# Kernel tuning notes

Measured on AMD Instinct MI355X. Metric: run time of the kernel, lower is better.

## Reference

```python
import jax, jax.numpy as jnp
import numpy as np

# ---- static config (mirrors TALoss(num_classes=80, reg_max=16, strides=[8,16,32])) ----
B, M, NC, REG_MAX = 32, 20, 80, 16
STRIDES = (8, 16, 32)
HW = ((80, 80), (40, 40), (20, 20))          # feature map sizes for 640x640 input
NO = REG_MAX * 4 + NC                         # 144 channels per head
A = sum(h * w for h, w in HW)                 # 8400 anchors
TOPK, ALPHA, BETA = 10, 0.5, 6.0
BOX_G, CLS_G, DFL_G = 7.5, 0.5, 1.5
EPS = 1e-9


def setup_inputs() -> dict:
    key = jax.random.key(0)
    ks = jax.random.split(key, 6)
    feats = {f"feat{i}": jax.random.normal(ks[i], (B, NO, h, w), jnp.float32)
             for i, (h, w) in enumerate(HW)}
    # targets: (N,6) rows of (img_idx, class, cx, cy, w, h), normalized, 20 boxes/image, sorted by image
    img_idx = jnp.repeat(jnp.arange(B, dtype=jnp.float32), M)
    cls = jax.random.randint(ks[3], (B * M,), 0, NC).astype(jnp.float32)
    cxy = jax.random.uniform(ks[4], (B * M, 2), minval=0.2, maxval=0.8)
    wh = jax.random.uniform(ks[5], (B * M, 2), minval=0.05, maxval=0.3)
    targets = jnp.concatenate([img_idx[:, None], cls[:, None], cxy, wh], axis=1)
    return {**feats, "targets": targets}


def _make_anchors():
    pts, strs = [], []
    for (h, w), s in zip(HW, STRIDES):
        sx = jnp.arange(w, dtype=jnp.float32) + 0.5
        sy = jnp.arange(h, dtype=jnp.float32) + 0.5
        gy, gx = jnp.meshgrid(sy, sx, indexing="ij")
        pts.append(jnp.stack([gx, gy], -1).reshape(-1, 2))
        strs.append(jnp.full((h * w, 1), float(s), jnp.float32))
    return jnp.concatenate(pts), jnp.concatenate(strs)   # (A,2), (A,1)


def _ciou(b1, b2, eps=1e-7):
    # b1, b2: broadcastable xyxy boxes (..., 4) -> CIoU (...,)
    b1x1, b1y1, b1x2, b1y2 = b1[..., 0], b1[..., 1], b1[..., 2], b1[..., 3]
    b2x1, b2y1, b2x2, b2y2 = b2[..., 0], b2[..., 1], b2[..., 2], b2[..., 3]
    w1, h1 = b1x2 - b1x1, b1y2 - b1y1 + eps
    w2, h2 = b2x2 - b2x1, b2y2 - b2y1 + eps
    inter = (jnp.clip(jnp.minimum(b1x2, b2x2) - jnp.maximum(b1x1, b2x1), 0)
             * jnp.clip(jnp.minimum(b1y2, b2y2) - jnp.maximum(b1y1, b2y1), 0))
    union = w1 * h1 + w2 * h2 - inter + eps
    iou = inter / union
    cw = jnp.maximum(b1x2, b2x2) - jnp.minimum(b1x1, b2x1)
    ch = jnp.maximum(b1y2, b2y2) - jnp.minimum(b1y1, b2y1)
    c2 = cw ** 2 + ch ** 2 + eps
    rho2 = ((b2x1 + b2x2 - b1x1 - b1x2) ** 2 + (b2y1 + b2y2 - b1y1 - b1y2) ** 2) / 4.0
    v = (4.0 / np.pi ** 2) * (jnp.arctan(w2 / h2) - jnp.arctan(w1 / h1)) ** 2
    a = jax.lax.stop_gradient(v / (v - iou + (1.0 + eps)))   # torch: computed under no_grad
    return iou - (rho2 / c2 + v * a)


def _assign(pd_scores, pd_bboxes, anc, gt_labels, gt_bboxes, mask_gt):
    """TaskAlignedAssigner. pd_scores (B,A,NC) sigmoid-ed, pd_bboxes (B,A,4) image units,
    anc (A,2) image units, gt_labels (B,M), gt_bboxes (B,M,4), mask_gt (B,M) float."""
    # anchors inside each gt box -> (B,M,A)
    lt = anc[None, None, :, :] - gt_bboxes[:, :, None, :2]
    rb = gt_bboxes[:, :, None, 2:] - anc[None, None, :, :]
    mask_in = (jnp.concatenate([lt, rb], -1).min(-1) > EPS).astype(jnp.float32)
    mask = mask_in * mask_gt[..., None]                      # (B,M,A) candidate mask
    overlaps = jnp.clip(_ciou(gt_bboxes[:, :, None, :], pd_bboxes[:, None, :, :]), 0) * mask
    labels = gt_labels.astype(jnp.int32)                     # (B,M)
    # scores of each gt's class at every anchor: (B,M,A)
    bbox_scores = jnp.take_along_axis(pd_scores.transpose(0, 2, 1),
                                      jnp.broadcast_to(labels[:, :, None], (B, M, A)), axis=1) * mask
    align = (bbox_scores ** ALPHA) * (overlaps ** BETA)      # (B,M,A), already zero off-mask
    # top-k anchors per gt
    _, idxs = jax.lax.top_k(align, TOPK)                     # (B,M,K)
    idxs = jnp.where(mask_gt[..., None] > 0, idxs, 0)
    cnt = jax.nn.one_hot(idxs, A, dtype=jnp.float32).sum(-2)  # (B,M,A)
    mask_topk = jnp.where(cnt > 1, 0.0, cnt)
    mask_pos = mask_topk * mask
    # resolve anchors matched to multiple gts: keep the max-overlap gt
    fg = mask_pos.sum(1)                                     # (B,A)
    is_max = jnp.moveaxis(jax.nn.one_hot(overlaps.argmax(1), M, dtype=jnp.float32), -1, 1)  # (B,M,A)
    mask_pos = jnp.where(fg[:, None, :] > 1, is_max, mask_pos)
    fg = mask_pos.sum(1)
    tgt_idx = mask_pos.argmax(1)                             # (B,A)
    t_labels = jnp.take_along_axis(labels, tgt_idx, 1)       # (B,A)
    t_bboxes = jnp.take_along_axis(gt_bboxes, tgt_idx[..., None], 1)  # (B,A,4)
    fg_b = (fg > 0).astype(jnp.float32)
    t_scores = jax.nn.one_hot(t_labels, NC, dtype=jnp.float32) * fg_b[..., None]
    # normalize scores: align * (max overlap per gt) / (max align per gt)
    align_pos = align * mask_pos
    pos_align = align_pos.max(-1, keepdims=True)             # (B,M,1)
    pos_over = (overlaps * mask_pos).max(-1, keepdims=True)
    norm = (align_pos * pos_over / (pos_align + EPS)).max(1)  # (B,A)
    return t_bboxes, t_scores * norm[..., None], fg_b


def _forward(feat0, feat1, feat2, targets):
    feats = [feat0, feat1, feat2]
    pred = jnp.concatenate([f.reshape(B, NO, -1) for f in feats], axis=2)
    pred_distri = pred[:, :REG_MAX * 4].transpose(0, 2, 1)   # (B,A,64)
    pred_scores = pred[:, REG_MAX * 4:].transpose(0, 2, 1)   # (B,A,NC)
    anc, stride_t = _make_anchors()
    img_h, img_w = HW[0][0] * STRIDES[0], HW[0][1] * STRIDES[0]
    scale = jnp.array([img_w, img_h, img_w, img_h], jnp.float32)
    # ---- preprocess targets (N,6) -> padded (B,M,5), xywh*scale -> xyxy ----
    idx = targets[:, 0].astype(jnp.int32)
    pos = jnp.arange(targets.shape[0]) - jnp.searchsorted(idx, idx, side="left")
    out = jnp.zeros((B, M, 5), jnp.float32).at[idx, pos].set(targets[:, 1:])
    gt_labels = out[..., 0]
    xywh = out[..., 1:5] * scale
    gt_bboxes = jnp.concatenate([xywh[..., :2] - xywh[..., 2:] / 2,
                                 xywh[..., :2] + xywh[..., 2:] / 2], -1)
    mask_gt = (gt_bboxes.sum(-1) > 0).astype(jnp.float32)    # (B,M)
    # ---- DFL bbox decode (feature-map units) ----
    proj = jnp.arange(REG_MAX, dtype=jnp.float32)
    dist = jax.nn.softmax(pred_distri.reshape(B, A, 4, REG_MAX), -1) @ proj  # (B,A,4) ltrb
    pred_bboxes = jnp.concatenate([anc - dist[..., :2], anc + dist[..., 2:]], -1)
    # ---- task-aligned assignment (on detached preds, image units) ----
    pd_scores = jax.lax.stop_gradient(jax.nn.sigmoid(pred_scores))
    pd_bboxes = jax.lax.stop_gradient(pred_bboxes) * stride_t
    target_bboxes, target_scores, fg_mask = _assign(pd_scores, pd_bboxes, anc * stride_t,
                                                    gt_labels, gt_bboxes, mask_gt)
    target_bboxes = target_bboxes / stride_t
    tss = jnp.maximum(target_scores.sum(), 1.0)
    # ---- BCE-with-logits classification loss (pos_weight=1) ----
    x, t = pred_scores, target_scores
    bce = jnp.maximum(x, 0) - x * t + jnp.log1p(jnp.exp(-jnp.abs(x)))
    loss_cls = bce.sum() / tss
    # ---- CIoU box loss + DFL, weighted by per-anchor target score sum on fg ----
    weight = target_scores.sum(-1) * fg_mask                 # (B,A)
    iou = _ciou(pred_bboxes, target_bboxes)
    loss_box = ((1.0 - iou) * weight).sum() / tss
    tltrb = jnp.clip(jnp.concatenate([anc - target_bboxes[..., :2],
                                      target_bboxes[..., 2:] - anc], -1),
                     0, REG_MAX - 1 - 0.01)                  # (B,A,4)
    logp = jax.nn.log_softmax(pred_distri.reshape(B, A, 4, REG_MAX), -1)
    tl = tltrb.astype(jnp.int32)
    wl = (tl + 1).astype(jnp.float32) - tltrb
    nll_l = -jnp.take_along_axis(logp, tl[..., None], -1)[..., 0]
    nll_r = -jnp.take_along_axis(logp, (tl + 1)[..., None], -1)[..., 0]
    dfl = (nll_l * wl + nll_r * (1.0 - wl)).mean(-1)         # (B,A)
    loss_dfl = (dfl * weight).sum() / tss
    losses = jnp.stack([loss_box * BOX_G, loss_cls * CLS_G, loss_dfl * DFL_G])
    return losses.sum() * B, jax.lax.stop_gradient(losses)


def reference(feat0, feat1, feat2, targets):
    return _forward(feat0, feat1, feat2, targets)
```

## Files before the change

### kernel.cpp

```cpp
#include <hip/hip_runtime.h>
#include <math.h>

constexpr int BB  = 32;
constexpr int MM  = 20;
constexpr int NCC = 80;
constexpr int RM  = 16;
constexpr int NOC = 144;
constexpr int AT  = 8400;
constexpr int TK  = 10;
constexpr int BA  = BB * AT;
constexpr int BM  = BB * MM;
constexpr int MAXPOS = BM * TK;
constexpr int NSLOT = 1024;
constexpr float EPS_A = 1e-9f;
constexpr float VCOEF = 0.40528473456935108577551785283891f;

constexpr int TPI    = 34;
constexpr int NTILES = BB * TPI;

struct Lvl { const float* f; int o, w, hw; float s; };

__device__ inline Lvl level_of(int a, const float* f0, const float* f1, const float* f2){
  Lvl L;
  if (a < 6400)      { L.f = f0; L.o = a;        L.w = 80; L.hw = 6400; L.s = 8.f;  }
  else if (a < 8000) { L.f = f1; L.o = a - 6400; L.w = 40; L.hw = 1600; L.s = 16.f; }
  else               { L.f = f2; L.o = a - 8000; L.w = 20; L.hw = 400;  L.s = 32.f; }
  return L;
}

__device__ inline float frcp(float x){ return __builtin_amdgcn_rcpf(x); }

__device__ inline float fast_atan(float x){
  float ax = fabsf(x);
  bool big = ax > 1.f;
  float z = big ? frcp(ax) : ax;
  float z2 = z * z;
  float p = fmaf(z2, -0.0117212f, 0.0526533f);
  p = fmaf(z2, p, -0.1164329f);
  p = fmaf(z2, p, 0.1935435f);
  p = fmaf(z2, p, -0.3326235f);
  p = fmaf(z2, p, 0.9999773f);
  float r = z * p;
  r = big ? 1.57079632679f - r : r;
  return copysignf(r, x);
}

__device__ inline float ciou_f(float b1x1,float b1y1,float b1x2,float b1y2,
                               float b2x1,float b2y1,float b2x2,float b2y2){
  const float eps = 1e-7f;
  float w1 = b1x2 - b1x1, h1 = b1y2 - b1y1 + eps;
  float w2 = b2x2 - b2x1, h2 = b2y2 - b2y1 + eps;
  float iw = fmaxf(fminf(b1x2, b2x2) - fmaxf(b1x1, b2x1), 0.f);
  float ih = fmaxf(fminf(b1y2, b2y2) - fmaxf(b1y1, b2y1), 0.f);
  float inter = iw * ih;
  float uni = w1 * h1 + w2 * h2 - inter + eps;
  float iou = inter * frcp(uni);
  float cw = fmaxf(b1x2, b2x2) - fminf(b1x1, b2x1);
  float ch = fmaxf(b1y2, b2y2) - fminf(b1y1, b2y1);
  float c2 = cw * cw + ch * ch + eps;
  float dx = b2x1 + b2x2 - b1x1 - b1x2;
  float dy = b2y1 + b2y2 - b1y1 - b1y2;
  float rho2 = (dx * dx + dy * dy) * 0.25f;
  float r1 = w1 * frcp(h1), r2 = w2 * frcp(h2);
  float dat = fast_atan((r2 - r1) * frcp(fmaf(r1, r2, 1.f)));
  float v = VCOEF * dat * dat;
  float alpha = v * frcp(v - iou + (1.0f + eps));
  return iou - (rho2 * frcp(c2) + v * alpha);
}

__device__ inline unsigned long long shfl_xor_u64(unsigned long long v, int mask){
  int lo = __shfl_xor((int)(unsigned)(v & 0xFFFFFFFFull), mask);
  int hi = __shfl_xor((int)(unsigned)(v >> 32), mask);
  return ((unsigned long long)(unsigned)hi << 32) | (unsigned)lo;
}

__device__ inline float softplus4(float4 v){
  float s = fmaxf(v.x, 0.f) + __logf(1.f + __expf(-fabsf(v.x)));
  s += fmaxf(v.y, 0.f) + __logf(1.f + __expf(-fabsf(v.y)));
  s += fmaxf(v.z, 0.f) + __logf(1.f + __expf(-fabsf(v.z)));
  s += fmaxf(v.w, 0.f) + __logf(1.f + __expf(-fabsf(v.w)));
  return s;
}

template<int NA, int HW, int W, int AOFF>
__device__ inline float feat_tile(const float* __restrict__ f, int b, int o0,
                                  float* __restrict__ sT,
                                  float4* __restrict__ pbox,
                                  float4* __restrict__ lse,
                                  unsigned* __restrict__ mpos){
  constexpr int NA4  = NA / 4;
  constexpr int NDF4 = 64 * NA4;
  constexpr int NIT  = NDF4 / 256;
  int tid = threadIdx.x;
  const float* base = f + (size_t)b * NOC * HW + o0;

  {
    float4 x[NIT];
#pragma unroll
    for (int k = 0; k < NIT; k++){
      int idx = k * 256 + tid;
      int ch = idx / NA4, pos = idx - ch * NA4;
      x[k] = *(const float4*)(base + (size_t)ch * HW + pos * 4);
    }
#pragma unroll
    for (int k = 0; k < NIT; k++){
      int idx = k * 256 + tid;
      int ch = idx / NA4, pos = idx - ch * NA4;
      *(float4*)(&sT[ch * NA + pos * 4]) = x[k];
    }
  }
  __syncthreads();

  if (tid < NA){
    float d[4], ls[4];
#pragma unroll
    for (int s = 0; s < 4; s++){
      float xs[16];
#pragma unroll
      for (int j = 0; j < 16; j++) xs[j] = sT[(s * 16 + j) * NA + tid];
      float mx = xs[0];
#pragma unroll
      for (int j = 1; j < 16; j++) mx = fmaxf(mx, xs[j]);
      float sm = 0.f, dt = 0.f;
#pragma unroll
      for (int j = 0; j < 16; j++){
        float e = __expf(xs[j] - mx);
        sm += e; dt = fmaf(e, (float)j, dt);
      }
      d[s]  = dt * frcp(sm);
      ls[s] = mx + __logf(sm);
    }
    int o = o0 + tid;
    int iy = o / W;
    float ax = (float)(o - iy * W) + 0.5f;
    float ay = (float)iy + 0.5f;
    int gi = b * AT + AOFF + o;
    pbox[gi] = make_float4(ax - d[0], ay - d[1], ax + d[2], ay + d[3]);
    lse[gi]  = make_float4(ls[0], ls[1], ls[2], ls[3]);
    mpos[gi] = 0u;
  }

  const float* cbase = base + (size_t)(4 * RM) * HW;
  constexpr int NCF4 = 80 * NA4;
  constexpr int NKC  = NCF4 / 256;
  float sp = 0.f;
#pragma unroll
  for (int k = 0; k < NKC; k++){
    int idx = k * 256 + tid;
    int ch = idx / NA4, pos = idx - ch * NA4;
    sp += softplus4(*(const float4*)(cbase + (size_t)ch * HW + pos * 4));
  }
  if constexpr (NCF4 % 256 != 0){
    int idx = NKC * 256 + tid;
    if (idx < NCF4){
      int ch = idx / NA4, pos = idx - ch * NA4;
      sp += softplus4(*(const float4*)(cbase + (size_t)ch * HW + pos * 4));
    }
  }
  return sp;
}

__global__ __launch_bounds__(256) void k_feat6(
    const float* __restrict__ f0, const float* __restrict__ f1,
    const float* __restrict__ f2, const float* __restrict__ tgt,
    float4* __restrict__ pbox, float4* __restrict__ lse,
    unsigned* __restrict__ mpos, double* __restrict__ bce_part,
    float* __restrict__ out5, float* __restrict__ gtbox,
    int* __restrict__ gtlab, float* __restrict__ gtmask,
    int* __restrict__ pa_i, int* __restrict__ po_i,
    int* __restrict__ topk_arr, double* __restrict__ acc){
  __shared__ float sT[64 * 256];
  __shared__ float red[4];
  int blk = blockIdx.x;
  int tid = threadIdx.x;
  if (blk < NTILES){
    int b = blk / TPI, tt = blk - b * TPI;
    float sp;
    if (tt < 25)       sp = feat_tile<256, 6400, 80, 0>   (f0, b, tt * 256,        sT, pbox, lse, mpos);
    else if (tt < 31)  sp = feat_tile<256, 1600, 40, 6400>(f1, b, (tt - 25) * 256, sT, pbox, lse, mpos);
    else if (tt == 31) sp = feat_tile< 64, 1600, 40, 6400>(f1, b, 1536,            sT, pbox, lse, mpos);
    else if (tt == 32) sp = feat_tile<256,  400, 20, 8000>(f2, b, 0,               sT, pbox, lse, mpos);
    else               sp = feat_tile<144,  400, 20, 8000>(f2, b, 256,             sT, pbox, lse, mpos);
    for (int off = 32; off; off >>= 1) sp += __shfl_down(sp, off);
    int wid = tid >> 6, lid = tid & 63;
    if (lid == 0) red[wid] = sp;
    __syncthreads();
    if (tid == 0) bce_part[blk] = (double)(red[0] + red[1] + red[2] + red[3]);
  } else {
    for (int i = tid; i < BM * 5; i += 256) out5[i] = 0.f;
    for (int i = tid; i < MAXPOS; i += 256) topk_arr[i] = -1;
    for (int i = tid; i < BM; i += 256){ pa_i[i] = 0; po_i[i] = 0; }
    if (tid < 8) acc[tid] = 0.0;
    __syncthreads();
    for (int t = tid; t < BM; t += 256){
      int img = (int)tgt[t * 6 + 0];
      int j = t;
      while (j > 0 && (int)tgt[(j - 1) * 6 + 0] == img) j--;
      int pos = t - j;
      if (img >= 0 && img < BB && pos < MM){
        for (int k = 0; k < 5; k++)
          out5[(img * MM + pos) * 5 + k] = tgt[t * 6 + 1 + k];
      }
    }
    __syncthreads();
    for (int t = tid; t < BM; t += 256){
      float lab = out5[t * 5 + 0];
      float cx = out5[t * 5 + 1] * 640.f;
      float cy = out5[t * 5 + 2] * 640.f;
      float w  = out5[t * 5 + 3] * 640.f;
      float h  = out5[t * 5 + 4] * 640.f;
      float x1 = cx - w * 0.5f, y1 = cy - h * 0.5f;
      float x2 = cx + w * 0.5f, y2 = cy + h * 0.5f;
      gtbox[t * 4 + 0] = x1; gtbox[t * 4 + 1] = y1;
      gtbox[t * 4 + 2] = x2; gtbox[t * 4 + 3] = y2;
      gtlab[t] = (int)lab;
      gtmask[t] = ((x1 + y1 + x2 + y2) > 0.f) ? 1.f : 0.f;
    }
  }
}

__global__ __launch_bounds__(256) void k_align(
    const float* __restrict__ f0, const float* __restrict__ f1,
    const float* __restrict__ f2, const float4* __restrict__ pbox,
    const float* __restrict__ gtbox, const int* __restrict__ gtlab,
    const float* __restrict__ gtmask,
    unsigned* __restrict__ mpos, int* __restrict__ topk_arr){
  int pair = blockIdx.x;
  int b = pair / MM, m = pair % MM;
  if (gtmask[pair] <= 0.f) return;
  int tid = threadIdx.x;
  float gx1 = gtbox[pair * 4 + 0], gy1 = gtbox[pair * 4 + 1];
  float gx2 = gtbox[pair * 4 + 2], gy2 = gtbox[pair * 4 + 3];
  int lab = gtlab[pair];
  __shared__ float s_val[NSLOT];
  __shared__ int   s_anc[NSLOT];
  __shared__ unsigned long long s_red[4];
  __shared__ int   s_win[TK];
  int base = 0;

#define PROC_LEVEL(FPTR, W, HW, AOFF, S)                                      \
  {                                                                           \
    const float s_ = (S); const float inv_ = 1.f / (S);                       \
    int x0 = max(0, (int)floorf(gx1 * inv_ - 0.5f));                          \
    int x1 = min((W) - 1, (int)ceilf(gx2 * inv_ - 0.5f));                     \
    int y0 = max(0, (int)floorf(gy1 * inv_ - 0.5f));                          \
    int y1 = min((W) - 1, (int)ceilf(gy2 * inv_ - 0.5f));                     \
    int nxx = x1 - x0 + 1, nyy = y1 - y0 + 1;                                 \
    if (nxx > 0 && nyy > 0){                                                  \
      int ntot = nxx * nyy;                                                   \
      unsigned magic = 0xFFFFFFFFu / (unsigned)nxx + 1u;                      \
      const float* clsrow = (FPTR) + (size_t)b * NOC * (HW)                   \
                            + (size_t)(4 * RM + lab) * (HW);                  \
      for (int t = tid; t < ntot; t += 256){                                  \
        int slot = base + t;                                                  \
        if (slot >= NSLOT) break;                                             \
        int iy = (int)(((unsigned long long)(unsigned)t * magic) >> 32);      \
        int ix = t - iy * nxx + x0;                                           \
        iy += y0;                                                             \
        float ax = ((float)ix + 0.5f) * s_;                                   \
        float ay = ((float)iy + 0.5f) * s_;                                   \
        float mn = fminf(fminf(ax - gx1, ay - gy1),                           \
                         fminf(gx2 - ax, gy2 - ay));                          \
        int o = iy * (W) + ix;                                                \
        int a = (AOFF) + o;                                                   \
        float aln = -1.f;                                                     \
        if (mn > EPS_A){                                                      \
          float4 pb = pbox[b * AT + a];                                       \
          float c = ciou_f(gx1, gy1, gx2, gy2,                                \
                           pb.x * s_, pb.y * s_, pb.z * s_, pb.w * s_);       \
          float ovl = fmaxf(c, 0.f);                                          \
          if (ovl > 0.f){                                                     \
            float xv = clsrow[o];                                             \
            float sc = frcp(1.f + __expf(-xv));                               \
            float o2 = ovl * ovl;                                             \
            aln = sqrtf(sc) * (o2 * o2 * o2);                                 \
          }                                                                   \
        }                                                                     \
        s_val[slot] = aln;                                                    \
        s_anc[slot] = a;                                                      \
      }                                                                       \
      base += ntot;                                                           \
    }                                                                         \
  }

  PROC_LEVEL(f0, 80, 6400, 0, 8.f)
  PROC_LEVEL(f1, 40, 1600, 6400, 16.f)
  PROC_LEVEL(f2, 20, 400, 8000, 32.f)
#undef PROC_LEVEL

  __syncthreads();
  int total = min(base, NSLOT);
  int wid = tid >> 6, lid = tid & 63;
  for (int r = 0; r < TK; r++){
    unsigned long long key = 0ULL;
    for (int i = tid; i < total; i += 256){
      float v = s_val[i];
      if (v > 0.f){
        unsigned long long k2 =
            ((unsigned long long)__float_as_uint(v) << 32) |
            (unsigned long long)(0xFFFFFFFFu - (unsigned)i);
        key = key > k2 ? key : k2;
      }
    }
    for (int xm = 1; xm < 64; xm <<= 1){
      unsigned long long o = shfl_xor_u64(key, xm);
      key = key > o ? key : o;
    }
    if (lid == 0) s_red[wid] = key;
    __syncthreads();
    if (tid == 0){
      unsigned long long k = s_red[0];
      k = k > s_red[1] ? k : s_red[1];
      k = k > s_red[2] ? k : s_red[2];
      k = k > s_red[3] ? k : s_red[3];
      if (k){
        int slot = (int)(0xFFFFFFFFu - (unsigned)(k & 0xFFFFFFFFull));
        s_win[r] = s_anc[slot];
        s_val[slot] = -1.f;
      } else s_win[r] = -1;
    }
    __syncthreads();
  }
  if (tid < TK){
    int a = s_win[tid];
    topk_arr[pair * TK + tid] = a;
    if (a >= 0) atomicOr(&mpos[(size_t)b * AT + a], 1u << m);
  }
}

__global__ __launch_bounds__(256) void k_resolve(
    const float* __restrict__ f0, const float* __restrict__ f1,
    const float* __restrict__ f2, const float4* __restrict__ pbox,
    const float* __restrict__ gtbox, const int* __restrict__ gtlab,
    const float* __restrict__ gtmask, const unsigned* __restrict__ mpos,
    const int* __restrict__ topk_arr,
    unsigned char* __restrict__ resm, float* __restrict__ resaln,
    int* __restrict__ pa_i, int* __restrict__ po_i){
  int i = blockIdx.x * 256 + threadIdx.x;
  int a = topk_arr[i];
  if (a < 0) return;
  int pair = i / TK;
  int b = pair / MM, m = pair % MM;
  unsigned bits = mpos[(size_t)b * AT + a];
  if (m != __ffs(bits) - 1) return;
  Lvl L = level_of(a, f0, f1, f2);
  float ax = ((float)(L.o % L.w) + 0.5f) * L.s;
  float ay = ((float)(L.o / L.w) + 0.5f) * L.s;
  float4 pb = pbox[b * AT + a];
  float px1 = pb.x * L.s, py1 = pb.y * L.s, px2 = pb.z * L.s, py2 = pb.w * L.s;
  int mr; float ovl;
  if (__popc(bits) > 1){
    float best = -1.f; int bm = 0;
    for (int mm = 0; mm < MM; mm++){
      float v = 0.f;
      if (gtmask[b * MM + mm] > 0.f){
        float x1 = gtbox[(b * MM + mm) * 4 + 0], y1 = gtbox[(b * MM + mm) * 4 + 1];
        float x2 = gtbox[(b * MM + mm) * 4 + 2], y2 = gtbox[(b * MM + mm) * 4 + 3];
        float mn = fminf(fminf(ax - x1, ay - y1), fminf(x2 - ax, y2 - ay));
        if (mn > EPS_A)
          v = fmaxf(ciou_f(x1, y1, x2, y2, px1, py1, px2, py2), 0.f);
      }
      if (v > best){ best = v; bm = mm; }
    }
    mr = bm; ovl = fmaxf(best, 0.f);
  } else {
    mr = m;
    float x1 = gtbox[(b * MM + mr) * 4 + 0], y1 = gtbox[(b * MM + mr) * 4 + 1];
    float x2 = gtbox[(b * MM + mr) * 4 + 2], y2 = gtbox[(b * MM + mr) * 4 + 3];
    ovl = fmaxf(ciou_f(x1, y1, x2, y2, px1, py1, px2, py2), 0.f);
  }
  int lab = gtlab[b * MM + mr];
  float xv = L.f[(size_t)b * NOC * L.hw + (size_t)(4 * RM + lab) * L.hw + L.o];
  float sc = frcp(1.f + __expf(-xv));
  float o2 = ovl * ovl;
  float aln = sqrtf(sc) * (o2 * o2 * o2);
  size_t gi = (size_t)b * AT + a;
  resm[gi] = (unsigned char)mr;
  resaln[gi] = aln;
  atomicMax(&pa_i[b * MM + mr], __float_as_int(aln));
  atomicMax(&po_i[b * MM + mr], __float_as_int(ovl));
}

__global__ __launch_bounds__(256) void k_final(
    const float* __restrict__ f0, const float* __restrict__ f1,
    const float* __restrict__ f2,
    const float4* __restrict__ pbox, const float4* __restrict__ lse,
    const float* __restrict__ gtbox, const int* __restrict__ gtlab,
    const int* __restrict__ pa_i, const int* __restrict__ po_i,
    const unsigned* __restrict__ mpos, const int* __restrict__ topk_arr,
    const unsigned char* __restrict__ resm, const float* __restrict__ resaln,
    double* __restrict__ acc){
  int i = blockIdx.x * 256 + threadIdx.x;
  float w_ = 0.f, clsp = 0.f, boxp = 0.f, dflp = 0.f;
  int a = topk_arr[i];
  if (a >= 0){
    int pair = i / TK;
    int b = pair / MM, m = pair % MM;
    unsigned bits = mpos[(size_t)b * AT + a];
    if (m == __ffs(bits) - 1){
      size_t gi = (size_t)b * AT + a;
      int mr = (int)resm[gi];
      float aln = resaln[gi];
      float pa = __int_as_float(pa_i[b * MM + mr]);
      float po = __int_as_float(po_i[b * MM + mr]);
      w_ = aln * po * frcp(pa + EPS_A);
      Lvl L = level_of(a, f0, f1, f2);
      const float* base = L.f + (size_t)b * NOC * L.hw + L.o;
      float ax = (float)(L.o % L.w) + 0.5f;
      float ay = (float)(L.o / L.w) + 0.5f;
      float inv_s = frcp(L.s);
      float tx1 = gtbox[(b * MM + mr) * 4 + 0] * inv_s, ty1 = gtbox[(b * MM + mr) * 4 + 1] * inv_s;
      float tx2 = gtbox[(b * MM + mr) * 4 + 2] * inv_s, ty2 = gtbox[(b * MM + mr) * 4 + 3] * inv_s;
      float4 pb = pbox[b * AT + a];
      float iou = ciou_f(pb.x, pb.y, pb.z, pb.w, tx1, ty1, tx2, ty2);
      boxp = (1.f - iou) * w_;
      float4 L4 = lse[b * AT + a];
      float lsv[4] = { L4.x, L4.y, L4.z, L4.w };
      float tv[4] = { ax - tx1, ay - ty1, tx2 - ax, ty2 - ay };
      float dfl = 0.f;
#pragma unroll
      for (int s4 = 0; s4 < 4; s4++){
        float t = fminf(fmaxf(tv[s4], 0.f), (float)(RM - 1) - 0.01f);
        int tl = (int)t;
        float wl = (float)(tl + 1) - t;
        float xl = base[(size_t)(s4 * RM + tl) * L.hw];
        float xr = base[(size_t)(s4 * RM + tl + 1) * L.hw];
        dfl += (lsv[s4] - xl) * wl + (lsv[s4] - xr) * (1.f - wl);
      }
      dflp = dfl * 0.25f * w_;
      int lab = gtlab[b * MM + mr];
      clsp = base[(size_t)(4 * RM + lab) * L.hw] * w_;
    }
  }
  __shared__ float red[4][4];
  float vals[4] = { w_, clsp, boxp, dflp };
  int wid = threadIdx.x >> 6, lid = threadIdx.x & 63;
#pragma unroll
  for (int j = 0; j < 4; j++){
    float v = vals[j];
    for (int off = 32; off; off >>= 1) v += __shfl_down(v, off);
    if (lid == 0) red[wid][j] = v;
  }
  __syncthreads();
  if (threadIdx.x == 0){
    float t0 = 0.f, t1 = 0.f, t2 = 0.f, t3 = 0.f;
    for (int w2 = 0; w2 < 4; w2++){
      t0 += red[w2][0]; t1 += red[w2][1]; t2 += red[w2][2]; t3 += red[w2][3];
    }
    atomicAdd(&acc[0], (double)t0);
    atomicAdd(&acc[1], (double)t1);
    atomicAdd(&acc[2], (double)t2);
    atomicAdd(&acc[3], (double)t3);
  }
}

__global__ void k_out(const double* __restrict__ acc,
                      const double* __restrict__ bce_part,
                      float* __restrict__ out){
  __shared__ double sd[256];
  double s = 0.0;
  for (int i = threadIdx.x; i < NTILES; i += 256) s += bce_part[i];
  sd[threadIdx.x] = s;
  __syncthreads();
  for (int off = 128; off; off >>= 1){
    if (threadIdx.x < off) sd[threadIdx.x] += sd[threadIdx.x + off];
    __syncthreads();
  }
  if (threadIdx.x == 0){
    double bce_sum = sd[0];
    double tss = acc[0] > 1.0 ? acc[0] : 1.0;
    double loss_box = acc[2] / tss;
    double loss_cls = (bce_sum - acc[1]) / tss;
    double loss_dfl = acc[3] / tss;
    float l0 = (float)(loss_box * 7.5);
    float l1 = (float)(loss_cls * 0.5);
    float l2 = (float)(loss_dfl * 1.5);
    out[0] = (l0 + l1 + l2) * 32.f;
    out[1] = l0;
    out[2] = l1;
    out[3] = l2;
  }
}

extern "C" void kernel_launch(void* const* d_in, const int* in_sizes, int n_in,
                              void* d_out, int out_size, void* d_ws, size_t ws_size,
                              hipStream_t stream) {
  const float* f0 = (const float*)d_in[0];
  const float* f1 = (const float*)d_in[1];
  const float* f2 = (const float*)d_in[2];
  const float* tg = (const float*)d_in[3];
  float* out = (float*)d_out;

  char* w = (char*)d_ws;
  size_t off = 0;
  auto alloc = [&](size_t bytes) -> void* {
    void* p = w + off;
    off += (bytes + 255) & ~(size_t)255;
    return p;
  };
  float4*        pbox    = (float4*)       alloc((size_t)BA * 16);
  float4*        lse     = (float4*)       alloc((size_t)BA * 16);
  float*         gtbox   = (float*)        alloc((size_t)BM * 16);
  int*           gtlab   = (int*)          alloc((size_t)BM * 4);
  float*         gtmask  = (float*)        alloc((size_t)BM * 4);
  float*         out5    = (float*)        alloc((size_t)BM * 20);
  unsigned*      mpos    = (unsigned*)     alloc((size_t)BA * 4);
  int*           topk_arr= (int*)          alloc((size_t)MAXPOS * 4);
  unsigned char* resm    = (unsigned char*)alloc((size_t)BA);
  float*         resaln  = (float*)        alloc((size_t)BA * 4);
  int*           pa      = (int*)          alloc((size_t)BM * 4);
  int*           po      = (int*)          alloc((size_t)BM * 4);
  double*        acc     = (double*)       alloc(8 * 8);
  double*        bcep    = (double*)       alloc((size_t)NTILES * 8);

  k_feat6<<<NTILES + 1, 256, 0, stream>>>(f0, f1, f2, tg, pbox, lse, mpos, bcep,
                                          out5, gtbox, gtlab, gtmask, pa, po,
                                          topk_arr, acc);
  k_align<<<BM, 256, 0, stream>>>(f0, f1, f2, pbox, gtbox, gtlab, gtmask, mpos, topk_arr);
  k_resolve<<<MAXPOS / 256, 256, 0, stream>>>(f0, f1, f2, pbox, gtbox, gtlab, gtmask,
                                              mpos, topk_arr, resm, resaln, pa, po);
  k_final<<<MAXPOS / 256, 256, 0, stream>>>(f0, f1, f2, pbox, lse, gtbox, gtlab,
                                            pa, po, mpos, topk_arr, resm, resaln, acc);
  k_out<<<1, 256, 0, stream>>>(acc, bcep, out);
}
```

Baseline: 248.5 us.

## Fuse align, resolve, final and output kernels into one persistent kernel with grid barriers

```diff
diff --git a/kernel.cpp b/kernel.cpp
--- a/kernel.cpp
+++ b/kernel.cpp
@@ -168,7 +168,7 @@
     float* __restrict__ out5, float* __restrict__ gtbox,
     int* __restrict__ gtlab, float* __restrict__ gtmask,
     int* __restrict__ pa_i, int* __restrict__ po_i,
-    int* __restrict__ topk_arr, double* __restrict__ acc){
+    int* __restrict__ topk_arr, int* __restrict__ bar){
   __shared__ float sT[64 * 256];
   __shared__ float red[4];
   int blk = blockIdx.x;
@@ -190,7 +190,7 @@
     for (int i = tid; i < BM * 5; i += 256) out5[i] = 0.f;
     for (int i = tid; i < MAXPOS; i += 256) topk_arr[i] = -1;
     for (int i = tid; i < BM; i += 256){ pa_i[i] = 0; po_i[i] = 0; }
-    if (tid < 8) acc[tid] = 0.0;
+    if (tid < 8) bar[tid] = 0;
     __syncthreads();
     for (int t = tid; t < BM; t += 256){
       int img = (int)tgt[t * 6 + 0];
@@ -219,24 +219,46 @@
   }
 }
 
-__global__ __launch_bounds__(256) void k_align(
+__device__ inline void grid_barrier(int* bar, int phase, int nblk){
+  __syncthreads();
+  if (threadIdx.x == 0){
+    __threadfence();
+    atomicAdd(&bar[phase], 1);
+    while (__hip_atomic_load(&bar[phase], __ATOMIC_ACQUIRE,
+                             __HIP_MEMORY_SCOPE_AGENT) < nblk){
+      __builtin_amdgcn_s_sleep(8);
+    }
+    __threadfence();
+  }
+  __syncthreads();
+}
+
+__global__ __launch_bounds__(256, 4) void k_tail(
     const float* __restrict__ f0, const float* __restrict__ f1,
     const float* __restrict__ f2, const float4* __restrict__ pbox,
+    const float4* __restrict__ lse,
     const float* __restrict__ gtbox, const int* __restrict__ gtlab,
     const float* __restrict__ gtmask,
-    unsigned* __restrict__ mpos, int* __restrict__ topk_arr){
-  int pair = blockIdx.x;
-  int b = pair / MM, m = pair % MM;
-  if (gtmask[pair] <= 0.f) return;
-  int tid = threadIdx.x;
-  float gx1 = gtbox[pair * 4 + 0], gy1 = gtbox[pair * 4 + 1];
-  float gx2 = gtbox[pair * 4 + 2], gy2 = gtbox[pair * 4 + 3];
-  int lab = gtlab[pair];
+    unsigned* __restrict__ mpos, int* __restrict__ topk_arr,
+    int* __restrict__ pa_i, int* __restrict__ po_i,
+    const double* __restrict__ bce_part, float* __restrict__ fpart,
+    int* __restrict__ bar, float* __restrict__ out){
   __shared__ float s_val[NSLOT];
   __shared__ int   s_anc[NSLOT];
   __shared__ unsigned long long s_red[4];
   __shared__ int   s_win[TK];
-  int base = 0;
+  __shared__ double sd[256];
+  __shared__ double res[5];
+
+  int pair = blockIdx.x;
+  int b = pair / MM, m = pair % MM;
+  int tid = threadIdx.x;
+
+  if (gtmask[pair] > 0.f){
+    float gx1 = gtbox[pair * 4 + 0], gy1 = gtbox[pair * 4 + 1];
+    float gx2 = gtbox[pair * 4 + 2], gy2 = gtbox[pair * 4 + 3];
+    int lab = gtlab[pair];
+    int base = 0;
 
 #define PROC_LEVEL(FPTR, W, HW, AOFF, S)                                      \
   {                                                                           \
@@ -283,129 +305,109 @@
     }                                                                         \
   }
 
-  PROC_LEVEL(f0, 80, 6400, 0, 8.f)
-  PROC_LEVEL(f1, 40, 1600, 6400, 16.f)
-  PROC_LEVEL(f2, 20, 400, 8000, 32.f)
+    PROC_LEVEL(f0, 80, 6400, 0, 8.f)
+    PROC_LEVEL(f1, 40, 1600, 6400, 16.f)
+    PROC_LEVEL(f2, 20, 400, 8000, 32.f)
 #undef PROC_LEVEL
 
-  __syncthreads();
-  int total = min(base, NSLOT);
-  int wid = tid >> 6, lid = tid & 63;
-  for (int r = 0; r < TK; r++){
-    unsigned long long key = 0ULL;
-    for (int i = tid; i < total; i += 256){
-      float v = s_val[i];
-      if (v > 0.f){
-        unsigned long long k2 =
-            ((unsigned long long)__float_as_uint(v) << 32) |
-            (unsigned long long)(0xFFFFFFFFu - (unsigned)i);
-        key = key > k2 ? key : k2;
-      }
-    }
-    for (int xm = 1; xm < 64; xm <<= 1){
-      unsigned long long o = shfl_xor_u64(key, xm);
-      key = key > o ? key : o;
-    }
-    if (lid == 0) s_red[wid] = key;
     __syncthreads();
-    if (tid == 0){
-      unsigned long long k = s_red[0];
-      k = k > s_red[1] ? k : s_red[1];
-      k = k > s_red[2] ? k : s_red[2];
-      k = k > s_red[3] ? k : s_red[3];
-      if (k){
-        int slot = (int)(0xFFFFFFFFu - (unsigned)(k & 0xFFFFFFFFull));
-        s_win[r] = s_anc[slot];
-        s_val[slot] = -1.f;
-      } else s_win[r] = -1;
-    }
-    __syncthreads();
-  }
+    int total = min(base, NSLOT);
+    int wid = tid >> 6, lid = tid & 63;
+    for (int r = 0; r < TK; r++){
+      unsigned long long key = 0ULL;
+      for (int i = tid; i < total; i += 256){
+        float v = s_val[i];
+        if (v > 0.f){
+          unsigned long long k2 =
+              ((unsigned long long)__float_as_uint(v) << 32) |
+              (unsigned long long)(0xFFFFFFFFu - (unsigned)i);
+          key = key > k2 ? key : k2;
+        }
+      }
+      for (int xm = 1; xm < 64; xm <<= 1){
+        unsigned long long o = shfl_xor_u64(key, xm);
+        key = key > o ? key : o;
+      }
+      if (lid == 0) s_red[wid] = key;
+      __syncthreads();
+      if (tid == 0){
+        unsigned long long k = s_red[0];
+        k = k > s_red[1] ? k : s_red[1];
+        k = k > s_red[2] ? k : s_red[2];
+        k = k > s_red[3] ? k : s_red[3];
+        if (k){
+          int slot = (int)(0xFFFFFFFFu - (unsigned)(k & 0xFFFFFFFFull));
+          s_win[r] = s_anc[slot];
+          s_val[slot] = -1.f;
+        } else s_win[r] = -1;
+      }
+      __syncthreads();
+    }
+    if (tid < TK){
+      int a = s_win[tid];
+      topk_arr[pair * TK + tid] = a;
+      if (a >= 0) atomicOr(&mpos[(size_t)b * AT + a], 1u << m);
+    }
+  }
+  grid_barrier(bar, 0, BM);
+
+  bool owner = false;
+  int a_own = -1, mr = 0;
+  float aln_own = 0.f;
   if (tid < TK){
-    int a = s_win[tid];
-    topk_arr[pair * TK + tid] = a;
-    if (a >= 0) atomicOr(&mpos[(size_t)b * AT + a], 1u << m);
-  }
-}
-
-__global__ __launch_bounds__(256) void k_resolve(
-    const float* __restrict__ f0, const float* __restrict__ f1,
-    const float* __restrict__ f2, const float4* __restrict__ pbox,
-    const float* __restrict__ gtbox, const int* __restrict__ gtlab,
-    const float* __restrict__ gtmask, const unsigned* __restrict__ mpos,
-    const int* __restrict__ topk_arr,
-    unsigned char* __restrict__ resm, float* __restrict__ resaln,
-    int* __restrict__ pa_i, int* __restrict__ po_i){
-  int i = blockIdx.x * 256 + threadIdx.x;
-  int a = topk_arr[i];
-  if (a < 0) return;
-  int pair = i / TK;
-  int b = pair / MM, m = pair % MM;
-  unsigned bits = mpos[(size_t)b * AT + a];
-  if (m != __ffs(bits) - 1) return;
-  Lvl L = level_of(a, f0, f1, f2);
-  float ax = ((float)(L.o % L.w) + 0.5f) * L.s;
-  float ay = ((float)(L.o / L.w) + 0.5f) * L.s;
-  float4 pb = pbox[b * AT + a];
-  float px1 = pb.x * L.s, py1 = pb.y * L.s, px2 = pb.z * L.s, py2 = pb.w * L.s;
-  int mr; float ovl;
-  if (__popc(bits) > 1){
-    float best = -1.f; int bm = 0;
-    for (int mm = 0; mm < MM; mm++){
-      float v = 0.f;
-      if (gtmask[b * MM + mm] > 0.f){
-        float x1 = gtbox[(b * MM + mm) * 4 + 0], y1 = gtbox[(b * MM + mm) * 4 + 1];
-        float x2 = gtbox[(b * MM + mm) * 4 + 2], y2 = gtbox[(b * MM + mm) * 4 + 3];
-        float mn = fminf(fminf(ax - x1, ay - y1), fminf(x2 - ax, y2 - ay));
-        if (mn > EPS_A)
-          v = fmaxf(ciou_f(x1, y1, x2, y2, px1, py1, px2, py2), 0.f);
-      }
-      if (v > best){ best = v; bm = mm; }
-    }
-    mr = bm; ovl = fmaxf(best, 0.f);
-  } else {
-    mr = m;
-    float x1 = gtbox[(b * MM + mr) * 4 + 0], y1 = gtbox[(b * MM + mr) * 4 + 1];
-    float x2 = gtbox[(b * MM + mr) * 4 + 2], y2 = gtbox[(b * MM + mr) * 4 + 3];
-    ovl = fmaxf(ciou_f(x1, y1, x2, y2, px1, py1, px2, py2), 0.f);
-  }
-  int lab = gtlab[b * MM + mr];
-  float xv = L.f[(size_t)b * NOC * L.hw + (size_t)(4 * RM + lab) * L.hw + L.o];
-  float sc = frcp(1.f + __expf(-xv));
-  float o2 = ovl * ovl;
-  float aln = sqrtf(sc) * (o2 * o2 * o2);
-  size_t gi = (size_t)b * AT + a;
-  resm[gi] = (unsigned char)mr;
-  resaln[gi] = aln;
-  atomicMax(&pa_i[b * MM + mr], __float_as_int(aln));
-  atomicMax(&po_i[b * MM + mr], __float_as_int(ovl));
-}
-
-__global__ __launch_bounds__(256) void k_final(
-    const float* __restrict__ f0, const float* __restrict__ f1,
-    const float* __restrict__ f2,
-    const float4* __restrict__ pbox, const float4* __restrict__ lse,
-    const float* __restrict__ gtbox, const int* __restrict__ gtlab,
-    const int* __restrict__ pa_i, const int* __restrict__ po_i,
-    const unsigned* __restrict__ mpos, const int* __restrict__ topk_arr,
-    const unsigned char* __restrict__ resm, const float* __restrict__ resaln,
-    double* __restrict__ acc){
-  int i = blockIdx.x * 256 + threadIdx.x;
-  float w_ = 0.f, clsp = 0.f, boxp = 0.f, dflp = 0.f;
-  int a = topk_arr[i];
-  if (a >= 0){
-    int pair = i / TK;
-    int b = pair / MM, m = pair % MM;
-    unsigned bits = mpos[(size_t)b * AT + a];
-    if (m == __ffs(bits) - 1){
-      size_t gi = (size_t)b * AT + a;
-      int mr = (int)resm[gi];
-      float aln = resaln[gi];
+    int i = pair * TK + tid;
+    int a = topk_arr[i];
+    if (a >= 0){
+      unsigned bits = mpos[(size_t)b * AT + a];
+      if (m == __ffs(bits) - 1){
+        owner = true; a_own = a;
+        Lvl L = level_of(a, f0, f1, f2);
+        float ax = ((float)(L.o % L.w) + 0.5f) * L.s;
+        float ay = ((float)(L.o / L.w) + 0.5f) * L.s;
+        float4 pb = pbox[b * AT + a];
+        float px1 = pb.x * L.s, py1 = pb.y * L.s, px2 = pb.z * L.s, py2 = pb.w * L.s;
+        float ovl;
+        if (__popc(bits) > 1){
+          float best = -1.f; int bm = 0;
+          for (int mm = 0; mm < MM; mm++){
+            float v = 0.f;
+            if (gtmask[b * MM + mm] > 0.f){
+              float x1 = gtbox[(b * MM + mm) * 4 + 0], y1 = gtbox[(b * MM + mm) * 4 + 1];
+              float x2 = gtbox[(b * MM + mm) * 4 + 2], y2 = gtbox[(b * MM + mm) * 4 + 3];
+              float mn = fminf(fminf(ax - x1, ay - y1), fminf(x2 - ax, y2 - ay));
+              if (mn > EPS_A)
+                v = fmaxf(ciou_f(x1, y1, x2, y2, px1, py1, px2, py2), 0.f);
+            }
+            if (v > best){ best = v; bm = mm; }
+          }
+          mr = bm; ovl = fmaxf(best, 0.f);
+        } else {
+          mr = m;
+          float x1 = gtbox[(b * MM + mr) * 4 + 0], y1 = gtbox[(b * MM + mr) * 4 + 1];
+          float x2 = gtbox[(b * MM + mr) * 4 + 2], y2 = gtbox[(b * MM + mr) * 4 + 3];
+          ovl = fmaxf(ciou_f(x1, y1, x2, y2, px1, py1, px2, py2), 0.f);
+        }
+        int lab = gtlab[b * MM + mr];
+        float xv = L.f[(size_t)b * NOC * L.hw + (size_t)(4 * RM + lab) * L.hw + L.o];
+        float sc = frcp(1.f + __expf(-xv));
+        float o2 = ovl * ovl;
+        aln_own = sqrtf(sc) * (o2 * o2 * o2);
+        atomicMax(&pa_i[b * MM + mr], __float_as_int(aln_own));
+        atomicMax(&po_i[b * MM + mr], __float_as_int(ovl));
+      }
+    }
+  }
+  grid_barrier(bar, 1, BM);
+
+  {
+    float w_ = 0.f, clsp = 0.f, boxp = 0.f, dflp = 0.f;
+    if (owner){
+      int a = a_own;
       float pa = __int_as_float(pa_i[b * MM + mr]);
       float po = __int_as_float(po_i[b * MM + mr]);
-      w_ = aln * po * frcp(pa + EPS_A);
+      w_ = aln_own * po * frcp(pa + EPS_A);
       Lvl L = level_of(a, f0, f1, f2);
-      const float* base = L.f + (size_t)b * NOC * L.hw + L.o;
+      const float* base2 = L.f + (size_t)b * NOC * L.hw + L.o;
       float ax = (float)(L.o % L.w) + 0.5f;
       float ay = (float)(L.o / L.w) + 0.5f;
       float inv_s = frcp(L.s);
@@ -423,62 +425,57 @@
         float t = fminf(fmaxf(tv[s4], 0.f), (float)(RM - 1) - 0.01f);
         int tl = (int)t;
         float wl = (float)(tl + 1) - t;
-        float xl = base[(size_t)(s4 * RM + tl) * L.hw];
-        float xr = base[(size_t)(s4 * RM + tl + 1) * L.hw];
+        float xl = base2[(size_t)(s4 * RM + tl) * L.hw];
+        float xr = base2[(size_t)(s4 * RM + tl + 1) * L.hw];
         dfl += (lsv[s4] - xl) * wl + (lsv[s4] - xr) * (1.f - wl);
       }
       dflp = dfl * 0.25f * w_;
       int lab = gtlab[b * MM + mr];
-      clsp = base[(size_t)(4 * RM + lab) * L.hw] * w_;
-    }
-  }
-  __shared__ float red[4][4];
-  float vals[4] = { w_, clsp, boxp, dflp };
-  int wid = threadIdx.x >> 6, lid = threadIdx.x & 63;
-#pragma unroll
-  for (int j = 0; j < 4; j++){
-    float v = vals[j];
-    for (int off = 32; off; off >>= 1) v += __shfl_down(v, off);
-    if (lid == 0) red[wid][j] = v;
-  }
-  __syncthreads();
-  if (threadIdx.x == 0){
-    float t0 = 0.f, t1 = 0.f, t2 = 0.f, t3 = 0.f;
-    for (int w2 = 0; w2 < 4; w2++){
-      t0 += red[w2][0]; t1 += red[w2][1]; t2 += red[w2][2]; t3 += red[w2][3];
-    }
-    atomicAdd(&acc[0], (double)t0);
-    atomicAdd(&acc[1], (double)t1);
-    atomicAdd(&acc[2], (double)t2);
-    atomicAdd(&acc[3], (double)t3);
-  }
-}
-
-__global__ void k_out(const double* __restrict__ acc,
-                      const double* __restrict__ bce_part,
-                      float* __restrict__ out){
-  __shared__ double sd[256];
-  double s = 0.0;
-  for (int i = threadIdx.x; i < NTILES; i += 256) s += bce_part[i];
-  sd[threadIdx.x] = s;
-  __syncthreads();
-  for (int off = 128; off; off >>= 1){
-    if (threadIdx.x < off) sd[threadIdx.x] += sd[threadIdx.x + off];
-    __syncthreads();
-  }
-  if (threadIdx.x == 0){
-    double bce_sum = sd[0];
-    double tss = acc[0] > 1.0 ? acc[0] : 1.0;
-    double loss_box = acc[2] / tss;
-    double loss_cls = (bce_sum - acc[1]) / tss;
-    double loss_dfl = acc[3] / tss;
-    float l0 = (float)(loss_box * 7.5);
-    float l1 = (float)(loss_cls * 0.5);
-    float l2 = (float)(loss_dfl * 1.5);
-    out[0] = (l0 + l1 + l2) * 32.f;
-    out[1] = l0;
-    out[2] = l1;
-    out[3] = l2;
+      clsp = base2[(size_t)(4 * RM + lab) * L.hw] * w_;
+    }
+    for (int off = 32; off; off >>= 1){
+      w_   += __shfl_down(w_, off);
+      clsp += __shfl_down(clsp, off);
+      boxp += __shfl_down(boxp, off);
+      dflp += __shfl_down(dflp, off);
+    }
+    if (tid == 0)
+      *(float4*)(&fpart[pair * 4]) = make_float4(w_, clsp, boxp, dflp);
+  }
+  grid_barrier(bar, 2, BM);
+
+  if (blockIdx.x == 0){
+    double part[5] = {0.0, 0.0, 0.0, 0.0, 0.0};
+    for (int i = tid; i < BM; i += 256){
+      float4 v = *(const float4*)(&fpart[i * 4]);
+      part[0] += (double)v.x; part[1] += (double)v.y;
+      part[2] += (double)v.z; part[3] += (double)v.w;
+    }
+    for (int i = tid; i < NTILES; i += 256) part[4] += bce_part[i];
+#pragma unroll
+    for (int j = 0; j < 5; j++){
+      sd[tid] = part[j];
+      __syncthreads();
+      for (int off = 128; off; off >>= 1){
+        if (tid < off) sd[tid] += sd[tid + off];
+        __syncthreads();
+      }
+      if (tid == 0) res[j] = sd[0];
+      __syncthreads();
+    }
+    if (tid == 0){
+      double tss = res[0] > 1.0 ? res[0] : 1.0;
+      double loss_box = res[2] / tss;
+      double loss_cls = (res[4] - res[1]) / tss;
+      double loss_dfl = res[3] / tss;
+      float l0 = (float)(loss_box * 7.5);
+      float l1 = (float)(loss_cls * 0.5);
+      float l2 = (float)(loss_dfl * 1.5);
+      out[0] = (l0 + l1 + l2) * 32.f;
+      out[1] = l0;
+      out[2] = l1;
+      out[3] = l2;
+    }
   }
 }
 
@@ -498,28 +495,23 @@
     off += (bytes + 255) & ~(size_t)255;
     return p;
   };
-  float4*        pbox    = (float4*)       alloc((size_t)BA * 16);
-  float4*        lse     = (float4*)       alloc((size_t)BA * 16);
-  float*         gtbox   = (float*)        alloc((size_t)BM * 16);
-  int*           gtlab   = (int*)          alloc((size_t)BM * 4);
-  float*         gtmask  = (float*)        alloc((size_t)BM * 4);
-  float*         out5    = (float*)        alloc((size_t)BM * 20);
-  unsigned*      mpos    = (unsigned*)     alloc((size_t)BA * 4);
-  int*           topk_arr= (int*)          alloc((size_t)MAXPOS * 4);
-  unsigned char* resm    = (unsigned char*)alloc((size_t)BA);
-  float*         resaln  = (float*)        alloc((size_t)BA * 4);
-  int*           pa      = (int*)          alloc((size_t)BM * 4);
-  int*           po      = (int*)          alloc((size_t)BM * 4);
-  double*        acc     = (double*)       alloc(8 * 8);
-  double*        bcep    = (double*)       alloc((size_t)NTILES * 8);
+  float4*   pbox    = (float4*)  alloc((size_t)BA * 16);
+  float4*   lse     = (float4*)  alloc((size_t)BA * 16);
+  float*    gtbox   = (float*)   alloc((size_t)BM * 16);
+  int*      gtlab   = (int*)     alloc((size_t)BM * 4);
+  float*    gtmask  = (float*)   alloc((size_t)BM * 4);
+  float*    out5    = (float*)   alloc((size_t)BM * 20);
+  unsigned* mpos    = (unsigned*)alloc((size_t)BA * 4);
+  int*      topk_arr= (int*)     alloc((size_t)MAXPOS * 4);
+  int*      pa      = (int*)     alloc((size_t)BM * 4);
+  int*      po      = (int*)     alloc((size_t)BM * 4);
+  double*   bcep    = (double*)  alloc((size_t)NTILES * 8);
+  float*    fpart   = (float*)   alloc((size_t)BM * 16);
+  int*      bar     = (int*)     alloc(8 * 4);
 
   k_feat6<<<NTILES + 1, 256, 0, stream>>>(f0, f1, f2, tg, pbox, lse, mpos, bcep,
                                           out5, gtbox, gtlab, gtmask, pa, po,
-                                          topk_arr, acc);
-  k_align<<<BM, 256, 0, stream>>>(f0, f1, f2, pbox, gtbox, gtlab, gtmask, mpos, topk_arr);
-  k_resolve<<<MAXPOS / 256, 256, 0, stream>>>(f0, f1, f2, pbox, gtbox, gtlab, gtmask,
-                                              mpos, topk_arr, resm, resaln, pa, po);
-  k_final<<<MAXPOS / 256, 256, 0, stream>>>(f0, f1, f2, pbox, lse, gtbox, gtlab,
-                                            pa, po, mpos, topk_arr, resm, resaln, acc);
-  k_out<<<1, 256, 0, stream>>>(acc, bcep, out);
-}
+                                          topk_arr, bar);
+  k_tail<<<BM, 256, 0, stream>>>(f0, f1, f2, pbox, lse, gtbox, gtlab, gtmask,
+                                 mpos, topk_arr, pa, po, bcep, fpart, bar, out);
+}
```

Result: slower. 472.9 us (+90.3%).
